# Kernel optimization log

Measured on AMD Instinct MI355X. Metric: run time of the kernel, lower is better.

Reference implementation:

```python
import jax, jax.numpy as jnp
import numpy as np

K = 8
NUM_BLOCKS = 4
ALPHA = K / (K + 1)  # 8/9


def _knn_norm_adj(xyz, k):
    """xyz: (B, 3, N) -> symmetric-normalized GCN adjacency (B, N, N).

    Mirrors knn_point(k, xyz, xyz) -> indices[:, 1:] -> get_adjacency_matrix,
    then the (input-independent) DenseGCNConv normalization: self loops set to 1,
    deg clamped >= 1, D^-1/2 A D^-1/2. adj is identical for every GCN call, so
    it is normalized once here.
    """
    x2 = jnp.sum(xyz * xyz, axis=1)                       # (B, N)
    inner = jnp.einsum('bci,bcj->bij', xyz, xyz)          # (B, N, N)
    dist = x2[:, :, None] + x2[:, None, :] - 2.0 * inner  # squared pairwise dist
    _, idx = jax.lax.top_k(-dist, k)                      # (B, N, k); self (dist 0) first
    nbr = idx[:, :, 1:]                                   # drop self -> k-1 neighbors
    B, N = x2.shape
    adj = jnp.zeros((B, N, N), xyz.dtype)
    adj = adj.at[jnp.arange(B)[:, None, None],
                 jnp.arange(N)[None, :, None], nbr].set(1.0)
    ar = jnp.arange(N)
    adj = adj.at[:, ar, ar].set(1.0)                      # add_loop=True
    dis = jnp.clip(jnp.sum(adj, axis=-1), 1.0, None) ** -0.5  # (B, N)
    return dis[:, :, None] * adj * dis[:, None, :]


def setup_inputs() -> dict:
    key = jax.random.key(0)
    ks = jax.random.split(key, 6)
    B, N, C = 16, 2048, 128
    s = 1.0 / np.sqrt(C).astype(np.float32)
    return {
        'xyz': jax.random.normal(ks[0], (B, 3, N), jnp.float32),
        'points': jax.random.normal(ks[1], (B, C, N), jnp.float32),
        'Wc': jax.random.normal(ks[2], (4, C, C), jnp.float32) * s,   # nn.Linear weights (out,in)
        'Wg': jax.random.normal(ks[3], (4, C, C), jnp.float32) * s,   # DenseGCNConv lin weights
        'Wuc': jax.random.normal(ks[4], (6, C), jnp.float32) * s,
        'Wug': jax.random.normal(ks[5], (6, C), jnp.float32) * s,
    }


def reference(xyz, points, Wc, Wg, Wuc, Wug):
    adj = _knn_norm_adj(xyz, K)                 # (B, N, N)
    pts = jnp.swapaxes(points, 1, 2)            # (B, N, C) channel-last internally
    for i in range(NUM_BLOCKS):
        shortcut = pts
        act = jax.nn.relu(pts)
        center = jnp.einsum('bnc,dc->bnd', act, Wc[i])                 # Linear on relu(points)
        grouped = adj @ jnp.einsum('bnc,dc->bnd', shortcut, Wg[i])     # DenseGCNConv on shortcut
        pts = (1.0 - ALPHA) * grouped + ALPHA * center + shortcut
    # unpool head
    points_xyz = jnp.einsum('bnd,od->bno', pts, Wuc)                   # (B, N, 6)
    grouped_xyz = adj @ jnp.einsum('bnd,od->bno', pts, Wug)            # (B, N, 6)
    new = ALPHA * points_xyz + (1.0 - ALPHA) * grouped_xyz
    B, N, _ = new.shape
    new = jnp.swapaxes(new, 1, 2).reshape(B, 3, 2, N) + xyz[:, :, None, :]
    new_xyz = new.reshape(B, 3, 2 * N)
    return new_xyz, jnp.swapaxes(pts, 1, 2)     # ((B,3,2N), (B,C,N))
```

## Files before the change

### kernel.cpp

```cpp
#include <hip/hip_runtime.h>
#include <hip/hip_bf16.h>

static constexpr int NB = 16;
static constexpr int NP = 2048;
static constexpr int NC = 128;
#define ALPHA_F ((float)(8.0/9.0))
#define OMA_F   ((float)(1.0 - 8.0/9.0))

typedef __attribute__((ext_vector_type(8))) short bfrag;
typedef __attribute__((ext_vector_type(4))) float ffrag;

union BU { bfrag v; uint4 u; unsigned int w[4]; };

__device__ inline void split2(float x, float y, unsigned& hi, unsigned& lo) {
    __hip_bfloat162 h = __float22bfloat162_rn(make_float2(x, y));
    float2 hb = __bfloat1622float2(h);
    __hip_bfloat162 l = __float22bfloat162_rn(make_float2(x - hb.x, y - hb.y));
    __builtin_memcpy(&hi, &h, 4);
    __builtin_memcpy(&lo, &l, 4);
}

__device__ inline void split1(float x, unsigned short& h, unsigned short& l) {
    __hip_bfloat16 hb = __float2bfloat16(x);
    float hf = __bfloat162float(hb);
    __hip_bfloat16 lb = __float2bfloat16(x - hf);
    __builtin_memcpy(&h, &hb, 2);
    __builtin_memcpy(&l, &lb, 2);
}

__global__ __launch_bounds__(256) void knn_kernel(const float* __restrict__ xyz,
                                                  int* __restrict__ nbr) {
    __shared__ float4 sp[NP];
    __shared__ float  md[64][33];
    __shared__ int    mi[64][33];
    int b = blockIdx.y;
    const float* X = xyz + (size_t)b * 3 * NP;
    for (int m = threadIdx.x; m < NP; m += 256) {
        float x = X[m], y = X[NP + m], z = X[2 * NP + m];
        sp[m ^ ((m >> 5) & 7)] = make_float4(x, y, z, x * x + y * y + z * z);
    }
    __syncthreads();

    int tid = threadIdx.x;
    int p = tid >> 2;
    int q = tid & 3;
    int base = blockIdx.x * 64;
    int n = base + p;
    float4 me = sp[n ^ ((n >> 5) & 7)];
    float xi = me.x, yi = me.y, zi = me.z, qi = me.w;

    unsigned gd[8];
#pragma unroll
    for (int t = 0; t < 8; ++t) gd[t] = 0x7F7FFFFFu;
#pragma unroll 1
    for (int gg = 0; gg < 16; ++gg) {
        int g = q * 16 + gg;
        const float4* gp = sp + g * 32;
        float m0 = 3.4e38f, m1 = m0, m2 = m0, m3 = m0;
#pragma unroll
        for (int k = 0; k < 32; k += 4) {
            float4 a0 = gp[(k + 0) ^ q];
            float4 a1 = gp[(k + 1) ^ q];
            float4 a2 = gp[(k + 2) ^ q];
            float4 a3 = gp[(k + 3) ^ q];
            m0 = fminf(m0, qi + a0.w - 2.0f * (xi * a0.x + yi * a0.y + zi * a0.z));
            m1 = fminf(m1, qi + a1.w - 2.0f * (xi * a1.x + yi * a1.y + zi * a1.z));
            m2 = fminf(m2, qi + a2.w - 2.0f * (xi * a2.x + yi * a2.y + zi * a2.z));
            m3 = fminf(m3, qi + a3.w - 2.0f * (xi * a3.x + yi * a3.y + zi * a3.z));
        }
        float gm = fmaxf(fminf(fminf(m0, m1), fminf(m2, m3)), 0.0f);
        unsigned pg; __builtin_memcpy(&pg, &gm, 4);
        pg = (pg & ~63u) | (unsigned)g;
        unsigned prev = gd[0];
        gd[0] = gd[0] < pg ? gd[0] : pg;
#pragma unroll
        for (int t = 1; t < 8; ++t) {
            unsigned mx = prev > pg ? prev : pg;
            prev = gd[t];
            gd[t] = gd[t] < mx ? gd[t] : mx;
        }
    }

#define CEU(A, B) { unsigned _lo = (A) < (B) ? (A) : (B); \
                    unsigned _hi = (A) < (B) ? (B) : (A); (A) = _lo; (B) = _hi; }
    unsigned cA[8];
#pragma unroll
    for (int i = 0; i < 8; ++i) {
        unsigned pb = (unsigned)__shfl_xor((int)gd[7 - i], 1);
        cA[i] = gd[i] < pb ? gd[i] : pb;
    }
    CEU(cA[0], cA[4]); CEU(cA[1], cA[5]); CEU(cA[2], cA[6]); CEU(cA[3], cA[7]);
    CEU(cA[0], cA[2]); CEU(cA[1], cA[3]); CEU(cA[4], cA[6]); CEU(cA[5], cA[7]);
    CEU(cA[0], cA[1]); CEU(cA[2], cA[3]); CEU(cA[4], cA[5]); CEU(cA[6], cA[7]);
    unsigned dA[8];
#pragma unroll
    for (int i = 0; i < 8; ++i) {
        unsigned pb = (unsigned)__shfl_xor((int)cA[7 - i], 2);
        dA[i] = cA[i] < pb ? cA[i] : pb;
    }
    unsigned long long mask = 0ull;
#pragma unroll
    for (int i = 0; i < 8; ++i) mask |= (1ull << (dA[i] & 63u));

    float bd[8]; int bi[8];
#pragma unroll
    for (int t = 0; t < 8; ++t) { bd[t] = 3.4e38f; bi[t] = 0; }
    while (mask) {
        int g = (int)__builtin_ctzll(mask);
        mask &= (mask - 1ull);
        int sw = g & 7;
        int jb = g * 32 + q;
#pragma unroll
        for (int i = 0; i < 8; ++i) {
            int j0 = jb + i * 4;
            float4 c4v = sp[j0 ^ sw];
            float inner = xi * c4v.x + yi * c4v.y + zi * c4v.z;
            float d = qi + c4v.w - 2.0f * inner;
            bool c[8];
#pragma unroll
            for (int t = 0; t < 8; ++t) c[t] = d < bd[t];
#pragma unroll
            for (int t = 7; t >= 1; --t) {
                bd[t] = c[t - 1] ? bd[t - 1] : (c[t] ? d : bd[t]);
                bi[t] = c[t - 1] ? bi[t - 1] : (c[t] ? j0 : bi[t]);
            }
            bd[0] = c[0] ? d : bd[0];
            bi[0] = c[0] ? j0 : bi[0];
        }
    }
#pragma unroll
    for (int t = 0; t < 8; ++t) {
        md[p][q * 8 + t] = bd[t];
        mi[p][q * 8 + t] = bi[t];
    }
    __syncthreads();

    if (tid < 64) {
        float fd[8]; int fi[8];
#pragma unroll
        for (int t = 0; t < 8; ++t) { fd[t] = 3.4e38f; fi[t] = 0; }
#pragma unroll 4
        for (int cc = 0; cc < 32; ++cc) {
            float d = md[tid][cc];
            int j = mi[tid][cc];
            bool c[8];
#pragma unroll
            for (int t = 0; t < 8; ++t) c[t] = d < fd[t];
#pragma unroll
            for (int t = 7; t >= 1; --t) {
                fd[t] = c[t - 1] ? fd[t - 1] : (c[t] ? d : fd[t]);
                fi[t] = c[t - 1] ? fi[t - 1] : (c[t] ? j : fi[t]);
            }
            fd[0] = c[0] ? d : fd[0];
            fi[0] = c[0] ? j : fi[0];
        }
        int row = b * NP + base + tid;
#pragma unroll
        for (int t = 0; t < 7; ++t) nbr[row * 7 + t] = fi[t + 1];
    }
}

__global__ __launch_bounds__(256) void prep_w_kernel(const float* __restrict__ Wc,
                                                     const float* __restrict__ Wg,
                                                     uint4* __restrict__ WP) {
    int t = blockIdx.x * 256 + threadIdx.x;
    int ncol = t & 127;
    int quad = (t >> 7) & 3;
    int s = (t >> 9) & 3;
    int mat = (t >> 11) & 1;
    int layer = t >> 12;
    const float* W = (mat ? Wg : Wc) + (size_t)layer * NC * NC + (size_t)ncol * NC + s * 32 + quad * 8;
    float4 a = *((const float4*)W);
    float4 b = *((const float4*)(W + 4));
    BU hi, lo;
    split2(a.x, a.y, hi.w[0], lo.w[0]);
    split2(a.z, a.w, hi.w[1], lo.w[1]);
    split2(b.x, b.y, hi.w[2], lo.w[2]);
    split2(b.z, b.w, hi.w[3], lo.w[3]);
    WP[t * 2] = hi.u;
    WP[t * 2 + 1] = lo.u;
}

template <int MODE>
__global__ __launch_bounds__(512, 4) void gemm_fused_kernel(const float* __restrict__ Asrc,
                                                            const float* __restrict__ Y2in,
                                                            const int* __restrict__ nbr,
                                                            const uint4* __restrict__ WPc,
                                                            const uint4* __restrict__ WPg,
                                                            float* __restrict__ Zout,
                                                            float* __restrict__ Y2out) {
    __shared__ unsigned short AhT[64][136];
    __shared__ unsigned short AlT[64][136];
    __shared__ int s_nb[448];
    int tid = threadIdx.x;
    int wid = tid >> 6, lane = tid & 63;
    int quad = lane >> 4, l15 = lane & 15;
    int xcd = blockIdx.x & 7;
    int slot = blockIdx.x >> 3;
    int bb = xcd * 2 + (slot >> 5);
    int n0 = (slot & 31) << 6;
    size_t m0 = (size_t)bb * NP + n0;
    int ncol = wid * 16 + l15;

    if (MODE == 1) {
        if (tid < 448) s_nb[tid] = nbr[m0 * 7 + tid];
        __syncthreads();
        size_t bbase = (size_t)bb * NP;
#pragma unroll 1
        for (int it = 0; it < 4; ++it) {
            int f = tid + it * 512;
            int r = f >> 5, c4 = (f & 31) * 4;
            size_t row = m0 + r;
            float4 z = *((const float4*)(Asrc + row * NC + c4));
            float4 acc = *((const float4*)(Y2in + row * NC + c4));
#pragma unroll
            for (int t = 0; t < 7; ++t) {
                int j = s_nb[r * 7 + t];
                float4 v = *((const float4*)(Y2in + (bbase + (size_t)j) * NC + c4));
                acc.x += v.x; acc.y += v.y; acc.z += v.z; acc.w += v.w;
            }
            float4 a;
            a.x = OMA_F * (0.125f * acc.x) + z.x;
            a.y = OMA_F * (0.125f * acc.y) + z.y;
            a.z = OMA_F * (0.125f * acc.z) + z.z;
            a.w = OMA_F * (0.125f * acc.w) + z.w;
            unsigned h01, l01, h23, l23;
            split2(a.x, a.y, h01, l01);
            split2(a.z, a.w, h23, l23);
            *((uint2*)&AhT[r][c4]) = make_uint2(h01, h23);
            *((uint2*)&AlT[r][c4]) = make_uint2(l01, l23);
        }
    } else {
#pragma unroll
        for (int it = 0; it < 4; ++it) {
            int f = tid + it * 512;
            int c = f >> 4, rq = (f & 15) * 4;
            float4 v = *((const float4*)(Asrc + ((size_t)bb * NC + c) * NP + n0 + rq));
            float vv[4] = {v.x, v.y, v.z, v.w};
#pragma unroll
            for (int k = 0; k < 4; ++k) {
                unsigned short h, l;
                split1(vv[k], h, l);
                AhT[rq + k][c] = h;
                AlT[rq + k][c] = l;
            }
        }
    }
    __syncthreads();

    BU Bch[4], Bcl[4], Bgh[4], Bgl[4];
#pragma unroll
    for (int s = 0; s < 4; ++s) {
        int idx = ((s * 4 + quad) * 128 + ncol) * 2;
        Bch[s].u = WPc[idx];
        Bcl[s].u = WPc[idx + 1];
        Bgh[s].u = WPg[idx];
        Bgl[s].u = WPg[idx + 1];
    }

    ffrag accC[4], accG[4];
#pragma unroll
    for (int mt = 0; mt < 4; ++mt) { accC[mt] = (ffrag)0.0f; accG[mt] = (ffrag)0.0f; }

#pragma unroll
    for (int s = 0; s < 4; ++s) {
#pragma unroll
        for (int mt = 0; mt < 4; ++mt) {
            int m = mt * 16 + l15;
            int k = s * 32 + quad * 8;
            BU ah, al, rh, rl;
            ah.u = *((const uint4*)&AhT[m][k]);
            al.u = *((const uint4*)&AlT[m][k]);
#pragma unroll
            for (int w = 0; w < 4; ++w) {
                unsigned msk = ((ah.w[w] & 0x80008000u) >> 15) * 0xFFFFu;
                rh.w[w] = ah.w[w] & ~msk;
                rl.w[w] = al.w[w] & ~msk;
            }
            accC[mt] = __builtin_amdgcn_mfma_f32_16x16x32_bf16(rh.v, Bch[s].v, accC[mt], 0, 0, 0);
            accC[mt] = __builtin_amdgcn_mfma_f32_16x16x32_bf16(rh.v, Bcl[s].v, accC[mt], 0, 0, 0);
            accC[mt] = __builtin_amdgcn_mfma_f32_16x16x32_bf16(rl.v, Bch[s].v, accC[mt], 0, 0, 0);
            accG[mt] = __builtin_amdgcn_mfma_f32_16x16x32_bf16(ah.v, Bgh[s].v, accG[mt], 0, 0, 0);
            accG[mt] = __builtin_amdgcn_mfma_f32_16x16x32_bf16(ah.v, Bgl[s].v, accG[mt], 0, 0, 0);
            accG[mt] = __builtin_amdgcn_mfma_f32_16x16x32_bf16(al.v, Bgh[s].v, accG[mt], 0, 0, 0);
        }
    }

#pragma unroll
    for (int mt = 0; mt < 4; ++mt) {
        int rbase = mt * 16 + quad * 4;
#pragma unroll
        for (int r = 0; r < 4; ++r) {
            int rr = rbase + r;
            unsigned hb = ((unsigned)AhT[rr][ncol]) << 16;
            unsigned lb = ((unsigned)AlT[rr][ncol]) << 16;
            float hp, lp;
            __builtin_memcpy(&hp, &hb, 4);
            __builtin_memcpy(&lp, &lb, 4);
            float p = hp + lp;
            size_t idx = (m0 + rr) * NC + ncol;
            Zout[idx] = p + ALPHA_F * accC[mt][r];
            Y2out[idx] = accG[mt][r];
        }
    }
}

__global__ __launch_bounds__(256) void agg2_kernel(const float* __restrict__ Z,
                                                   const float* __restrict__ Y2,
                                                   const int* __restrict__ nbr,
                                                   const float* __restrict__ Wuc,
                                                   const float* __restrict__ Wug,
                                                   float* __restrict__ U,
                                                   float* __restrict__ out2) {
    __shared__ float s1[6 * NC], s2[6 * NC];
    __shared__ float sm[8][132];
    int tid = threadIdx.x;
    int lane = tid & 31, rl = tid >> 5;
    for (int m = tid; m < 6 * NC; m += 256) { s1[m] = Wuc[m]; s2[m] = Wug[m]; }

    int xcd = blockIdx.x & 7;
    int slot = blockIdx.x >> 3;
    int bb = xcd * 2 + (slot >> 8);
    int rblk = slot & 255;
    int n0 = rblk * 8;
    size_t row = ((size_t)bb << 11) + n0 + rl;
    const int* nb = nbr + row * 7;
    size_t off = row * NC + lane * 4;
    float4 ys = *((const float4*)(Y2 + off));
    size_t bbase = (size_t)bb * NP * NC;
#pragma unroll
    for (int t = 0; t < 7; ++t) {
        int j = nb[t];
        float4 v = *((const float4*)(Y2 + bbase + (size_t)j * NC + lane * 4));
        ys.x += v.x; ys.y += v.y; ys.z += v.z; ys.w += v.w;
    }
    float4 z = *((const float4*)(Z + off));
    float4 o;
    o.x = OMA_F * (0.125f * ys.x) + z.x;
    o.y = OMA_F * (0.125f * ys.y) + z.y;
    o.z = OMA_F * (0.125f * ys.z) + z.z;
    o.w = OMA_F * (0.125f * ys.w) + z.w;

    __syncthreads();
    *((float4*)&sm[rl][lane * 4]) = o;

    float a1[6], a2[6];
#pragma unroll
    for (int oo = 0; oo < 6; ++oo) {
        float4 w1 = *((const float4*)&s1[oo * NC + lane * 4]);
        float4 w2 = *((const float4*)&s2[oo * NC + lane * 4]);
        a1[oo] = o.x * w1.x + o.y * w1.y + o.z * w1.z + o.w * w1.w;
        a2[oo] = o.x * w2.x + o.y * w2.y + o.z * w2.z + o.w * w2.w;
    }
#pragma unroll
    for (int s = 1; s < 32; s <<= 1) {
#pragma unroll
        for (int oo = 0; oo < 6; ++oo) {
            a1[oo] += __shfl_xor(a1[oo], s);
            a2[oo] += __shfl_xor(a2[oo], s);
        }
    }
    if (lane == 0) {
        float* Ur = U + row * 12;
        float4 u0 = make_float4(a1[0], a1[1], a1[2], a1[3]);
        float4 u1 = make_float4(a1[4], a1[5], a2[0], a2[1]);
        float4 u2 = make_float4(a2[2], a2[3], a2[4], a2[5]);
        *((float4*)(Ur + 0)) = u0;
        *((float4*)(Ur + 4)) = u1;
        *((float4*)(Ur + 8)) = u2;
    }

    __syncthreads();
    int c = tid >> 1, h = tid & 1;
    float4 v;
    v.x = sm[4 * h + 0][c];
    v.y = sm[4 * h + 1][c];
    v.z = sm[4 * h + 2][c];
    v.w = sm[4 * h + 3][c];
    *((float4*)(out2 + ((size_t)bb * NC + c) * NP + n0 + 4 * h)) = v;
}

__global__ __launch_bounds__(256) void final_out_kernel(const float* __restrict__ U,
                                                        const int* __restrict__ nbr,
                                                        const float* __restrict__ xyz,
                                                        float* __restrict__ out) {
    size_t row = (size_t)blockIdx.x * 256 + threadIdx.x;
    int b = (int)(row >> 11), n = (int)(row & 2047);
    const int* nb = nbr + row * 7;
    float u1[6], u2[6];
#pragma unroll
    for (int o = 0; o < 6; ++o) { u1[o] = U[row * 12 + o]; u2[o] = U[row * 12 + 6 + o]; }
#pragma unroll
    for (int t = 0; t < 7; ++t) {
        int j = nb[t];
        const float* Uj = U + ((size_t)b * NP + j) * 12 + 6;
#pragma unroll
        for (int o = 0; o < 6; ++o) u2[o] += Uj[o];
    }
#pragma unroll
    for (int c = 0; c < 3; ++c)
#pragma unroll
        for (int s = 0; s < 2; ++s) {
            int o = c * 2 + s;
            float val = ALPHA_F * u1[o] + OMA_F * (0.125f * u2[o])
                      + xyz[(size_t)b * 3 * NP + (size_t)c * NP + n];
            out[(size_t)b * 3 * 2 * NP + (size_t)c * 2 * NP + (size_t)s * NP + n] = val;
        }
}

extern "C" void kernel_launch(void* const* d_in, const int* in_sizes, int n_in,
                              void* d_out, int out_size, void* d_ws, size_t ws_size,
                              hipStream_t stream) {
    const float* xyz    = (const float*)d_in[0];
    const float* points = (const float*)d_in[1];
    const float* Wc     = (const float*)d_in[2];
    const float* Wg     = (const float*)d_in[3];
    const float* Wuc    = (const float*)d_in[4];
    const float* Wug    = (const float*)d_in[5];
    float* out = (float*)d_out;

    char* ws = (char*)d_ws;
    size_t o = 0;
    int* nbr  = (int*)(ws + o);     o += (size_t)NB * NP * 7 * 4;
    uint4* WP = (uint4*)(ws + o);   o += (size_t)32768 * 16;
    float* Za = (float*)(ws + o);   o += (size_t)NB * NP * NC * 4;
    float* Ya = (float*)(ws + o);   o += (size_t)NB * NP * NC * 4;
    float* Zb = (float*)(ws + o);   o += (size_t)NB * NP * NC * 4;
    float* Yb = (float*)(ws + o);   o += (size_t)NB * NP * NC * 4;
    float* U  = (float*)(ws + o);   o += (size_t)NB * NP * 12 * 4;

    const int GEMM_GRID = NB * NP / 64;
    #define WPC(L) (WP + (size_t)((L) * 2 + 0) * 4096)
    #define WPG(L) (WP + (size_t)((L) * 2 + 1) * 4096)

    prep_w_kernel<<<64, 256, 0, stream>>>(Wc, Wg, WP);
    knn_kernel<<<dim3(NP / 64, NB), 256, 0, stream>>>(xyz, nbr);
    gemm_fused_kernel<0><<<GEMM_GRID, 512, 0, stream>>>(points, nullptr, nullptr,
        WPC(0), WPG(0), Za, Ya);
    gemm_fused_kernel<1><<<GEMM_GRID, 512, 0, stream>>>(Za, Ya, nbr,
        WPC(1), WPG(1), Zb, Yb);
    gemm_fused_kernel<1><<<GEMM_GRID, 512, 0, stream>>>(Zb, Yb, nbr,
        WPC(2), WPG(2), Za, Ya);
    gemm_fused_kernel<1><<<GEMM_GRID, 512, 0, stream>>>(Za, Ya, nbr,
        WPC(3), WPG(3), Zb, Yb);
    float* out2 = out + (size_t)NB * 3 * 2 * NP;
    agg2_kernel<<<dim3(NB * NP / 8), 256, 0, stream>>>(Zb, Yb, nbr, Wuc, Wug, U, out2);
    final_out_kernel<<<dim3(NB * NP / 256), 256, 0, stream>>>(U, nbr, xyz, out);
}
```

Measured before the change: 197.3 us.

## Fuse GCN layers and unpool head into one persistent cooperative kernel

```diff
diff --git a/kernel.cpp b/kernel.cpp
--- a/kernel.cpp
+++ b/kernel.cpp
@@ -1,5 +1,8 @@
 #include <hip/hip_runtime.h>
 #include <hip/hip_bf16.h>
+#include <hip/hip_cooperative_groups.h>
+
+namespace cg = cooperative_groups;
 
 static constexpr int NB = 16;
 static constexpr int NP = 2048;
@@ -26,6 +29,15 @@
     __hip_bfloat16 lb = __float2bfloat16(x - hf);
     __builtin_memcpy(&h, &hb, 2);
     __builtin_memcpy(&l, &lb, 2);
+}
+
+__device__ inline float2 pair2f(unsigned hu, unsigned lu) {
+    unsigned hx = (hu & 0xFFFFu) << 16, hy = hu & 0xFFFF0000u;
+    unsigned lx = (lu & 0xFFFFu) << 16, ly = lu & 0xFFFF0000u;
+    float fhx, fhy, flx, fly;
+    __builtin_memcpy(&fhx, &hx, 4); __builtin_memcpy(&fhy, &hy, 4);
+    __builtin_memcpy(&flx, &lx, 4); __builtin_memcpy(&fly, &ly, 4);
+    return make_float2(fhx + flx, fhy + fly);
 }
 
 __global__ __launch_bounds__(256) void knn_kernel(const float* __restrict__ xyz,
@@ -179,6 +191,269 @@
     split2(b.z, b.w, hi.w[3], lo.w[3]);
     WP[t * 2] = hi.u;
     WP[t * 2 + 1] = lo.u;
+}
+
+__device__ __forceinline__ void mfma_layer(const uint4* __restrict__ WPc,
+                                           const uint4* __restrict__ WPg,
+                                           unsigned short (&AhT)[64][136],
+                                           unsigned short (&AlT)[64][136],
+                                           float* __restrict__ yout,
+                                           size_t m0, int quad, int l15, int ncol) {
+    BU Bch[4], Bcl[4], Bgh[4], Bgl[4];
+#pragma unroll
+    for (int s = 0; s < 4; ++s) {
+        int idx = ((s * 4 + quad) * 128 + ncol) * 2;
+        Bch[s].u = WPc[idx];
+        Bcl[s].u = WPc[idx + 1];
+        Bgh[s].u = WPg[idx];
+        Bgl[s].u = WPg[idx + 1];
+    }
+    ffrag accC[4], accG[4];
+#pragma unroll
+    for (int mt = 0; mt < 4; ++mt) { accC[mt] = (ffrag)0.0f; accG[mt] = (ffrag)0.0f; }
+#pragma unroll
+    for (int s = 0; s < 4; ++s) {
+#pragma unroll
+        for (int mt = 0; mt < 4; ++mt) {
+            int m = mt * 16 + l15;
+            int k = s * 32 + quad * 8;
+            BU ah, al, rh, rl;
+            ah.u = *((const uint4*)&AhT[m][k]);
+            al.u = *((const uint4*)&AlT[m][k]);
+#pragma unroll
+            for (int w = 0; w < 4; ++w) {
+                unsigned msk = ((ah.w[w] & 0x80008000u) >> 15) * 0xFFFFu;
+                rh.w[w] = ah.w[w] & ~msk;
+                rl.w[w] = al.w[w] & ~msk;
+            }
+            accC[mt] = __builtin_amdgcn_mfma_f32_16x16x32_bf16(rh.v, Bch[s].v, accC[mt], 0, 0, 0);
+            accC[mt] = __builtin_amdgcn_mfma_f32_16x16x32_bf16(rh.v, Bcl[s].v, accC[mt], 0, 0, 0);
+            accC[mt] = __builtin_amdgcn_mfma_f32_16x16x32_bf16(rl.v, Bch[s].v, accC[mt], 0, 0, 0);
+            accG[mt] = __builtin_amdgcn_mfma_f32_16x16x32_bf16(ah.v, Bgh[s].v, accG[mt], 0, 0, 0);
+            accG[mt] = __builtin_amdgcn_mfma_f32_16x16x32_bf16(ah.v, Bgl[s].v, accG[mt], 0, 0, 0);
+            accG[mt] = __builtin_amdgcn_mfma_f32_16x16x32_bf16(al.v, Bgh[s].v, accG[mt], 0, 0, 0);
+        }
+    }
+    __syncthreads();
+#pragma unroll
+    for (int mt = 0; mt < 4; ++mt) {
+        int rbase = mt * 16 + quad * 4;
+#pragma unroll
+        for (int r = 0; r < 4; ++r) {
+            int rr = rbase + r;
+            unsigned hb = ((unsigned)AhT[rr][ncol]) << 16;
+            unsigned lb = ((unsigned)AlT[rr][ncol]) << 16;
+            float hp, lp;
+            __builtin_memcpy(&hp, &hb, 4);
+            __builtin_memcpy(&lp, &lb, 4);
+            float z = (hp + lp) + ALPHA_F * accC[mt][r];
+            unsigned short zh, zl;
+            split1(z, zh, zl);
+            AhT[rr][ncol] = zh;
+            AlT[rr][ncol] = zl;
+            yout[(m0 + rr) * NC + ncol] = accG[mt][r];
+        }
+    }
+}
+
+__global__ __launch_bounds__(512, 4) void gcn_persistent_kernel(
+        const float* __restrict__ points,
+        const int* __restrict__ nbr,
+        const uint4* __restrict__ WP,
+        const float* __restrict__ Wuc,
+        const float* __restrict__ Wug,
+        const float* __restrict__ xyz,
+        float* __restrict__ Ya,
+        float* __restrict__ Yb,
+        float* __restrict__ U,
+        float* __restrict__ out) {
+    cg::grid_group grid = cg::this_grid();
+
+    __shared__ unsigned short AhT[64][136];
+    __shared__ unsigned short AlT[64][136];
+    __shared__ int   s_nb[448];
+    __shared__ float sW[12 * NC];
+
+    int tid = threadIdx.x;
+    int wid = tid >> 6, lane = tid & 63;
+    int quad = lane >> 4, l15 = lane & 15;
+    int xcd = blockIdx.x & 7;
+    int slot = blockIdx.x >> 3;
+    int bb = xcd * 2 + (slot >> 5);
+    int n0 = (slot & 31) << 6;
+    size_t m0 = (size_t)bb * NP + n0;
+    size_t bbase = (size_t)bb * NP;
+    int ncol = wid * 16 + l15;
+
+    if (tid < 448) s_nb[tid] = nbr[m0 * 7 + tid];
+    for (int m = tid; m < 12 * NC; m += 512)
+        sW[m] = (m < 6 * NC) ? Wuc[m] : Wug[m - 6 * NC];
+
+#pragma unroll
+    for (int it = 0; it < 4; ++it) {
+        int f = tid + it * 512;
+        int c = f >> 4, rq = (f & 15) * 4;
+        float4 v = *((const float4*)(points + ((size_t)bb * NC + c) * NP + n0 + rq));
+        float vv[4] = {v.x, v.y, v.z, v.w};
+#pragma unroll
+        for (int k = 0; k < 4; ++k) {
+            unsigned short h, l;
+            split1(vv[k], h, l);
+            AhT[rq + k][c] = h;
+            AlT[rq + k][c] = l;
+        }
+    }
+    __syncthreads();
+    mfma_layer(WP, WP + 4096, AhT, AlT, Ya, m0, quad, l15, ncol);
+    grid.sync();
+
+#pragma unroll 1
+    for (int L = 1; L < 4; ++L) {
+        const float* yin  = (L & 1) ? Ya : Yb;
+        float*       yout = (L & 1) ? Yb : Ya;
+        const uint4* WPc = WP + (size_t)(L * 2 + 0) * 4096;
+        const uint4* WPg = WP + (size_t)(L * 2 + 1) * 4096;
+
+#pragma unroll 1
+        for (int it = 0; it < 4; ++it) {
+            int f = tid + it * 512;
+            int r = f >> 5, c4 = (f & 31) * 4;
+            size_t row = m0 + r;
+            float4 acc = *((const float4*)(yin + row * NC + c4));
+#pragma unroll
+            for (int t = 0; t < 7; ++t) {
+                int j = s_nb[r * 7 + t];
+                float4 v = *((const float4*)(yin + (bbase + (size_t)j) * NC + c4));
+                acc.x += v.x; acc.y += v.y; acc.z += v.z; acc.w += v.w;
+            }
+            uint2 hu = *((const uint2*)&AhT[r][c4]);
+            uint2 lu = *((const uint2*)&AlT[r][c4]);
+            float2 z01 = pair2f(hu.x, lu.x);
+            float2 z23 = pair2f(hu.y, lu.y);
+            float4 a;
+            a.x = OMA_F * (0.125f * acc.x) + z01.x;
+            a.y = OMA_F * (0.125f * acc.y) + z01.y;
+            a.z = OMA_F * (0.125f * acc.z) + z23.x;
+            a.w = OMA_F * (0.125f * acc.w) + z23.y;
+            unsigned h01, l01, h23, l23;
+            split2(a.x, a.y, h01, l01);
+            split2(a.z, a.w, h23, l23);
+            *((uint2*)&AhT[r][c4]) = make_uint2(h01, h23);
+            *((uint2*)&AlT[r][c4]) = make_uint2(l01, l23);
+        }
+        __syncthreads();
+        mfma_layer(WPc, WPg, AhT, AlT, yout, m0, quad, l15, ncol);
+        grid.sync();
+    }
+
+#pragma unroll 1
+    for (int it = 0; it < 4; ++it) {
+        int f = tid + it * 512;
+        int r = f >> 5, c4 = (f & 31) * 4;
+        size_t row = m0 + r;
+        float4 ys = *((const float4*)(Yb + row * NC + c4));
+#pragma unroll
+        for (int t = 0; t < 7; ++t) {
+            int j = s_nb[r * 7 + t];
+            float4 v = *((const float4*)(Yb + (bbase + (size_t)j) * NC + c4));
+            ys.x += v.x; ys.y += v.y; ys.z += v.z; ys.w += v.w;
+        }
+        uint2 hu = *((const uint2*)&AhT[r][c4]);
+        uint2 lu = *((const uint2*)&AlT[r][c4]);
+        float2 z01 = pair2f(hu.x, lu.x);
+        float2 z23 = pair2f(hu.y, lu.y);
+        float4 o;
+        o.x = OMA_F * (0.125f * ys.x) + z01.x;
+        o.y = OMA_F * (0.125f * ys.y) + z01.y;
+        o.z = OMA_F * (0.125f * ys.z) + z23.x;
+        o.w = OMA_F * (0.125f * ys.w) + z23.y;
+        unsigned h01, l01, h23, l23;
+        split2(o.x, o.y, h01, l01);
+        split2(o.z, o.w, h23, l23);
+        *((uint2*)&AhT[r][c4]) = make_uint2(h01, h23);
+        *((uint2*)&AlT[r][c4]) = make_uint2(l01, l23);
+    }
+    __syncthreads();
+
+    {
+        int row = tid >> 3, k = tid & 7;
+        float a1[6] = {0, 0, 0, 0, 0, 0}, a2[6] = {0, 0, 0, 0, 0, 0};
+#pragma unroll
+        for (int i = 0; i < 4; ++i) {
+            int c4 = k * 16 + i * 4;
+            uint2 hu = *((const uint2*)&AhT[row][c4]);
+            uint2 lu = *((const uint2*)&AlT[row][c4]);
+            float2 p01 = pair2f(hu.x, lu.x);
+            float2 p23 = pair2f(hu.y, lu.y);
+#pragma unroll
+            for (int oo = 0; oo < 6; ++oo) {
+                float4 w1 = *((const float4*)&sW[oo * NC + c4]);
+                float4 w2 = *((const float4*)&sW[(6 + oo) * NC + c4]);
+                a1[oo] += p01.x * w1.x + p01.y * w1.y + p23.x * w1.z + p23.y * w1.w;
+                a2[oo] += p01.x * w2.x + p01.y * w2.y + p23.x * w2.z + p23.y * w2.w;
+            }
+        }
+#pragma unroll
+        for (int s = 1; s < 8; s <<= 1) {
+#pragma unroll
+            for (int oo = 0; oo < 6; ++oo) {
+                a1[oo] += __shfl_xor(a1[oo], s);
+                a2[oo] += __shfl_xor(a2[oo], s);
+            }
+        }
+        if (k == 0) {
+            float* Ur = U + (m0 + row) * 12;
+            *((float4*)(Ur + 0)) = make_float4(a1[0], a1[1], a1[2], a1[3]);
+            *((float4*)(Ur + 4)) = make_float4(a1[4], a1[5], a2[0], a2[1]);
+            *((float4*)(Ur + 8)) = make_float4(a2[2], a2[3], a2[4], a2[5]);
+        }
+    }
+
+    {
+        float* out2 = out + (size_t)NB * 3 * 2 * NP;
+#pragma unroll
+        for (int it = 0; it < 4; ++it) {
+            int u = tid + it * 512;
+            int c = u >> 4, nseg = (u & 15) * 4;
+            float4 v;
+#pragma unroll
+            for (int j = 0; j < 4; ++j) {
+                unsigned hb = ((unsigned)AhT[nseg + j][c]) << 16;
+                unsigned lb = ((unsigned)AlT[nseg + j][c]) << 16;
+                float hp, lp;
+                __builtin_memcpy(&hp, &hb, 4);
+                __builtin_memcpy(&lp, &lb, 4);
+                ((float*)&v)[j] = hp + lp;
+            }
+            *((float4*)(out2 + ((size_t)bb * NC + c) * NP + n0 + nseg)) = v;
+        }
+    }
+    grid.sync();
+
+    if (tid < 64) {
+        size_t row = m0 + tid;
+        int n = n0 + tid;
+        const int* nb = s_nb + tid * 7;
+        float u1[6], u2[6];
+#pragma unroll
+        for (int o = 0; o < 6; ++o) { u1[o] = U[row * 12 + o]; u2[o] = U[row * 12 + 6 + o]; }
+#pragma unroll
+        for (int t = 0; t < 7; ++t) {
+            int j = nb[t];
+            const float* Uj = U + (bbase + (size_t)j) * 12 + 6;
+#pragma unroll
+            for (int o = 0; o < 6; ++o) u2[o] += Uj[o];
+        }
+#pragma unroll
+        for (int c = 0; c < 3; ++c)
+#pragma unroll
+            for (int s = 0; s < 2; ++s) {
+                int o = c * 2 + s;
+                float val = ALPHA_F * u1[o] + OMA_F * (0.125f * u2[o])
+                          + xyz[(size_t)bb * 3 * NP + (size_t)c * NP + n];
+                out[(size_t)bb * 3 * 2 * NP + (size_t)c * 2 * NP + (size_t)s * NP + n] = val;
+            }
+    }
 }
 
 template <int MODE>
@@ -362,12 +637,9 @@
     }
     if (lane == 0) {
         float* Ur = U + row * 12;
-        float4 u0 = make_float4(a1[0], a1[1], a1[2], a1[3]);
-        float4 u1 = make_float4(a1[4], a1[5], a2[0], a2[1]);
-        float4 u2 = make_float4(a2[2], a2[3], a2[4], a2[5]);
-        *((float4*)(Ur + 0)) = u0;
-        *((float4*)(Ur + 4)) = u1;
-        *((float4*)(Ur + 8)) = u2;
+        *((float4*)(Ur + 0)) = make_float4(a1[0], a1[1], a1[2], a1[3]);
+        *((float4*)(Ur + 4)) = make_float4(a1[4], a1[5], a2[0], a2[1]);
+        *((float4*)(Ur + 8)) = make_float4(a2[2], a2[3], a2[4], a2[5]);
     }
 
     __syncthreads();
@@ -435,15 +707,23 @@
 
     prep_w_kernel<<<64, 256, 0, stream>>>(Wc, Wg, WP);
     knn_kernel<<<dim3(NP / 64, NB), 256, 0, stream>>>(xyz, nbr);
-    gemm_fused_kernel<0><<<GEMM_GRID, 512, 0, stream>>>(points, nullptr, nullptr,
-        WPC(0), WPG(0), Za, Ya);
-    gemm_fused_kernel<1><<<GEMM_GRID, 512, 0, stream>>>(Za, Ya, nbr,
-        WPC(1), WPG(1), Zb, Yb);
-    gemm_fused_kernel<1><<<GEMM_GRID, 512, 0, stream>>>(Zb, Yb, nbr,
-        WPC(2), WPG(2), Za, Ya);
-    gemm_fused_kernel<1><<<GEMM_GRID, 512, 0, stream>>>(Za, Ya, nbr,
-        WPC(3), WPG(3), Zb, Yb);
-    float* out2 = out + (size_t)NB * 3 * 2 * NP;
-    agg2_kernel<<<dim3(NB * NP / 8), 256, 0, stream>>>(Zb, Yb, nbr, Wuc, Wug, U, out2);
-    final_out_kernel<<<dim3(NB * NP / 256), 256, 0, stream>>>(U, nbr, xyz, out);
-}
+
+    void* args[] = {(void*)&points, (void*)&nbr, (void*)&WP, (void*)&Wuc,
+                    (void*)&Wug, (void*)&xyz, (void*)&Ya, (void*)&Yb,
+                    (void*)&U, (void*)&out};
+    hipError_t e = hipLaunchCooperativeKernel((void*)gcn_persistent_kernel,
+                                              dim3(512), dim3(512), args, 0, stream);
+    if (e != hipSuccess) {
+        float* out2 = out + (size_t)NB * 3 * 2 * NP;
+        gemm_fused_kernel<0><<<GEMM_GRID, 512, 0, stream>>>(points, nullptr, nullptr,
+            WPC(0), WPG(0), Za, Ya);
+        gemm_fused_kernel<1><<<GEMM_GRID, 512, 0, stream>>>(Za, Ya, nbr,
+            WPC(1), WPG(1), Zb, Yb);
+        gemm_fused_kernel<1><<<GEMM_GRID, 512, 0, stream>>>(Zb, Yb, nbr,
+            WPC(2), WPG(2), Za, Ya);
+        gemm_fused_kernel<1><<<GEMM_GRID, 512, 0, stream>>>(Za, Ya, nbr,
+            WPC(3), WPG(3), Zb, Yb);
+        agg2_kernel<<<dim3(NB * NP / 8), 256, 0, stream>>>(Zb, Yb, nbr, Wuc, Wug, U, out2);
+        final_out_kernel<<<dim3(NB * NP / 256), 256, 0, stream>>>(U, nbr, xyz, out);
+    }
+}
```

Result: slower. 512.5 us (+159.8%).
